# Optimization experiments

Measured on AMD Instinct MI355X. Metric: run time of the kernel, lower is better.

Reference implementation:

```python
import jax, jax.numpy as jnp
import numpy as np

D_K = 64.0  # key size from init


def setup_inputs() -> dict:
    key = jax.random.key(0)
    k1, k2, k3, k4, k5 = jax.random.split(key, 5)
    B, H, S, D = 2, 16, 2048, 64
    q = jax.random.normal(k1, (B, H, S, D), dtype=jnp.float32)
    v = jax.random.normal(k2, (B, H, S, D), dtype=jnp.float32)
    k = jax.random.normal(k3, (B, H, S, D), dtype=jnp.float32)
    att_mask = jax.random.normal(k4, (B, 1, S, S), dtype=jnp.float32)
    seq_mask = jax.random.uniform(k5, (B, 1, 1, S), dtype=jnp.float32)
    return {"q": q, "v": v, "k": k, "att_mask": att_mask, "seq_mask": seq_mask}


def reference(q, v, k, att_mask, seq_mask):
    # scores: [B, H, S, S]
    scores = jnp.einsum("bhqd,bhkd->bhqk", q, k) / jnp.sqrt(jnp.asarray(D_K, q.dtype))
    scores = scores + att_mask
    weights = jax.nn.softmax(scores, axis=-1)
    weights = weights * seq_mask  # post-softmax mask, no renormalization
    out = jnp.einsum("bhqk,bhkd->bhqd", weights, v)
    return out
```

## Files before the change

### kernel.cpp

```cpp
#include <hip/hip_runtime.h>
#include <hip/hip_bf16.h>
#include <stdint.h>

typedef __attribute__((ext_vector_type(8)))  short    short8;
typedef __attribute__((ext_vector_type(4)))  float    floatx4;
typedef __attribute__((ext_vector_type(16))) float    floatx16;
typedef __attribute__((ext_vector_type(4)))  ushort   ushortx4;

static __device__ __forceinline__ ushort f2bf(float f) {
  union { float f; uint32_t u; } c;
  c.f = f;
  uint32_t u = c.u;
  uint32_t r = (u + 0x7FFFu + ((u >> 16) & 1u)) >> 16;
  return (ushort)r;
}

static __device__ __forceinline__ uint32_t pkbf(float a, float b) {
  return (uint32_t)f2bf(a) | ((uint32_t)f2bf(b) << 16);
}

static __device__ __forceinline__ short8 pack8(floatx4 a, floatx4 b) {
  short8 t;
  t[0] = (short)f2bf(a[0]); t[1] = (short)f2bf(a[1]);
  t[2] = (short)f2bf(a[2]); t[3] = (short)f2bf(a[3]);
  t[4] = (short)f2bf(b[0]); t[5] = (short)f2bf(b[1]);
  t[6] = (short)f2bf(b[2]); t[7] = (short)f2bf(b[3]);
  return t;
}

#define MFMA32(a, b, c) __builtin_amdgcn_mfma_f32_32x32x16_bf16((a), (b), (c), 0, 0, 0)

constexpr int S_LEN = 2048;
constexpr int DH    = 64;
constexpr int QBLK  = 128;
constexpr int KVBLK = 64;
constexpr int NT    = S_LEN / KVBLK;

static __device__ __forceinline__ void swap32(uint32_t& a, uint32_t& b, int hi) {
#if __has_builtin(__builtin_amdgcn_permlane32_swap)
  typedef int intx2 __attribute__((ext_vector_type(2)));
  intx2 r = __builtin_amdgcn_permlane32_swap((int)a, (int)b, false, false);
  a = (uint32_t)r[0]; b = (uint32_t)r[1];
#else
  uint32_t pa = (uint32_t)__shfl_xor((int)a, 32, 64);
  uint32_t pb = (uint32_t)__shfl_xor((int)b, 32, 64);
  uint32_t na = hi ? pb : a;
  uint32_t nb = hi ? b  : pa;
  a = na; b = nb;
#endif
}

__global__ __launch_bounds__(256, 2)
void attn_fwd(const float* __restrict__ Q, const float* __restrict__ V,
              const float* __restrict__ K, const float* __restrict__ AM,
              const float* __restrict__ SM, float* __restrict__ O)
{
  __shared__ ushort Kl[2][KVBLK * DH];
  __shared__ ushort Vt[2][DH * KVBLK];
  __shared__ float  smlds[S_LEN];

  const int bh   = blockIdx.x;
  const int qt   = blockIdx.y;
  const int tid  = threadIdx.x;
  const int lane = tid & 63;
  const int wave = tid >> 6;
  const int l31  = lane & 31;
  const int hi   = lane >> 5;

  const float* qptr  = Q  + (size_t)bh * S_LEN * DH;
  const float* kptr  = K  + (size_t)bh * S_LEN * DH;
  const float* vptr  = V  + (size_t)bh * S_LEN * DH;
  const float* amptr = AM + (size_t)(bh >> 4) * S_LEN * S_LEN;
  const float* smptr = SM + (size_t)(bh >> 4) * S_LEN;
  float* optr = O + (size_t)bh * S_LEN * DH;

  for (int i = tid; i < S_LEN / 4; i += 256)
    ((floatx4*)smlds)[i] = ((const floatx4*)smptr)[i];

  const int qw = qt * QBLK + wave * 32;

  short8 qf[4];
  {
    const float* p = qptr + (size_t)(qw + l31) * DH + hi * 8;
    #pragma unroll
    for (int s = 0; s < 4; ++s) {
      floatx4 f0 = *(const floatx4*)(p + s * 16);
      floatx4 f1 = *(const floatx4*)(p + s * 16 + 4);
      qf[s] = pack8(f0, f1);
    }
  }

  const int krow = tid >> 2;
  const int kcol = (tid & 3) * 16;
  const int kcb  = (tid & 3) * 2;
  const int vr0  = (tid & 15) * 4;
  const int vd0  = (tid >> 4) * 4;

  floatx4 kreg[4], vreg[4];
  floatx4 amreg[2][4], amnx[2][4];

  auto LOADKV = [&](int t) {
    const float* kg = kptr + (size_t)(t * KVBLK + krow) * DH + kcol;
    #pragma unroll
    for (int j = 0; j < 4; ++j) kreg[j] = ((const floatx4*)kg)[j];
    #pragma unroll
    for (int i = 0; i < 4; ++i)
      vreg[i] = *(const floatx4*)(vptr + (size_t)(t * KVBLK + vr0 + i) * DH + vd0);
  };

  auto WRITEKV = [&](int c) {
    const int sw = krow & 7;
    *(short8*)&Kl[c][krow * 64 + ((kcb ^ sw) * 8)]       = pack8(kreg[0], kreg[1]);
    *(short8*)&Kl[c][krow * 64 + (((kcb + 1) ^ sw) * 8)] = pack8(kreg[2], kreg[3]);
    #pragma unroll
    for (int d = 0; d < 4; ++d) {
      ushortx4 w;
      w[0] = f2bf(vreg[0][d]); w[1] = f2bf(vreg[1][d]);
      w[2] = f2bf(vreg[2][d]); w[3] = f2bf(vreg[3][d]);
      const int row = vd0 + d;
      const int ch  = (vr0 >> 3) ^ (row & 7);
      *(ushortx4*)&Vt[c][row * 64 + ch * 8 + (vr0 & 7)] = w;
    }
  };

  auto LOADAM = [&](int t, floatx4 am[2][4]) {
    const float* base = amptr + (size_t)(qw + l31) * S_LEN + t * KVBLK + hi * 4;
    #pragma unroll
    for (int blk = 0; blk < 2; ++blk)
      #pragma unroll
      for (int j = 0; j < 4; ++j)
        am[blk][j] = *(const floatx4*)(base + blk * 32 + j * 8);
  };

  LOADKV(0);
  WRITEKV(0);
  LOADAM(0, amreg);

  float m_run = -3.0e38f, l_run = 0.f;
  floatx16 oacc[2];
  #pragma unroll
  for (int db = 0; db < 2; ++db)
    #pragma unroll
    for (int r = 0; r < 16; ++r) oacc[db][r] = 0.f;

  #pragma unroll 1
  for (int t = 0; t < NT; ++t) {
    const int c = t & 1;
    __syncthreads();

    floatx16 sacc[2];
    #pragma unroll
    for (int blk = 0; blk < 2; ++blk) {
      #pragma unroll
      for (int r = 0; r < 16; ++r) sacc[blk][r] = 0.f;
      const int row = blk * 32 + l31;
      const int sw  = row & 7;
      #pragma unroll
      for (int s = 0; s < 4; ++s) {
        const int ch = (s * 2 + hi) ^ sw;
        short8 kf = *(const short8*)&Kl[c][row * 64 + ch * 8];
        sacc[blk] = MFMA32(kf, qf[s], sacc[blk]);
      }
    }

    float p[2][16];
    float pmax = -3.0e38f;
    #pragma unroll
    for (int blk = 0; blk < 2; ++blk)
      #pragma unroll
      for (int r = 0; r < 16; ++r) {
        const float v = fmaf(sacc[blk][r], 0.125f, amreg[blk][r >> 2][r & 3]);
        p[blk][r] = v;
        pmax = fmaxf(pmax, v);
      }
    pmax = fmaxf(pmax, __shfl_xor(pmax, 32, 64));

    if (__any(pmax > m_run)) {
      const float mnew = fmaxf(m_run, pmax);
      const float fac  = __expf(m_run - mnew);
      float fw[16];
      #pragma unroll
      for (int r = 0; r < 16; ++r)
        fw[r] = __shfl(fac, (r & 3) + 8 * (r >> 2) + 4 * hi, 64);
      #pragma unroll
      for (int db = 0; db < 2; ++db)
        #pragma unroll
        for (int r = 0; r < 16; ++r) oacc[db][r] *= fw[r];
      l_run *= fac;
      m_run = mnew;
    }

    float ssum = 0.f;
    #pragma unroll
    for (int blk = 0; blk < 2; ++blk)
      #pragma unroll
      for (int r = 0; r < 16; ++r) {
        const float e = __expf(p[blk][r] - m_run);
        p[blk][r] = e;
        ssum += e;
      }
    ssum += __shfl_xor(ssum, 32, 64);
    l_run += ssum;

    const bool pf = (t + 1 < NT);
    if (pf) { LOADKV(t + 1); LOADAM(t + 1, amnx); }

    floatx4 smv[2][4];
    #pragma unroll
    for (int blk = 0; blk < 2; ++blk)
      #pragma unroll
      for (int j = 0; j < 4; ++j)
        smv[blk][j] = *(const floatx4*)&smlds[t * KVBLK + blk * 32 + hi * 4 + j * 8];

    uint32_t pw[2][2][4];
    #pragma unroll
    for (int blk = 0; blk < 2; ++blk)
      #pragma unroll
      for (int ks = 0; ks < 2; ++ks) {
        float q0 = p[blk][ks * 8 + 0] * smv[blk][ks * 2 + 0][0];
        float q1 = p[blk][ks * 8 + 1] * smv[blk][ks * 2 + 0][1];
        float q2 = p[blk][ks * 8 + 2] * smv[blk][ks * 2 + 0][2];
        float q3 = p[blk][ks * 8 + 3] * smv[blk][ks * 2 + 0][3];
        float q4 = p[blk][ks * 8 + 4] * smv[blk][ks * 2 + 1][0];
        float q5 = p[blk][ks * 8 + 5] * smv[blk][ks * 2 + 1][1];
        float q6 = p[blk][ks * 8 + 6] * smv[blk][ks * 2 + 1][2];
        float q7 = p[blk][ks * 8 + 7] * smv[blk][ks * 2 + 1][3];
        uint32_t w0 = pkbf(q0, q1);
        uint32_t w1 = pkbf(q2, q3);
        uint32_t w2 = pkbf(q4, q5);
        uint32_t w3 = pkbf(q6, q7);
        swap32(w0, w2, hi);
        swap32(w1, w3, hi);
        pw[blk][ks][0] = w0; pw[blk][ks][1] = w1;
        pw[blk][ks][2] = w2; pw[blk][ks][3] = w3;
      }

    #pragma unroll
    for (int blk = 0; blk < 2; ++blk)
      #pragma unroll
      for (int ks = 0; ks < 2; ++ks) {
        union { uint32_t u[4]; short8 s; } af;
        af.u[0] = pw[blk][ks][0]; af.u[1] = pw[blk][ks][1];
        af.u[2] = pw[blk][ks][2]; af.u[3] = pw[blk][ks][3];
        #pragma unroll
        for (int db = 0; db < 2; ++db) {
          const int row = db * 32 + l31;
          const int ch  = (blk * 4 + ks * 2 + hi) ^ (row & 7);
          short8 vf = *(const short8*)&Vt[c][row * 64 + ch * 8];
          oacc[db] = MFMA32(af.s, vf, oacc[db]);
        }
      }

    if (pf) {
      WRITEKV(c ^ 1);
      #pragma unroll
      for (int blk = 0; blk < 2; ++blk)
        #pragma unroll
        for (int j = 0; j < 4; ++j) amreg[blk][j] = amnx[blk][j];
    }
  }

  const float inv = 1.0f / l_run;
  float iw[16];
  #pragma unroll
  for (int r = 0; r < 16; ++r)
    iw[r] = __shfl(inv, (r & 3) + 8 * (r >> 2) + 4 * hi, 64);
  #pragma unroll
  for (int db = 0; db < 2; ++db)
    #pragma unroll
    for (int r = 0; r < 16; ++r) {
      const int qr = (r & 3) + 8 * (r >> 2) + 4 * hi;
      optr[(size_t)(qw + qr) * DH + db * 32 + l31] = oacc[db][r] * iw[r];
    }
}

extern "C" void kernel_launch(void* const* d_in, const int* in_sizes, int n_in,
                              void* d_out, int out_size, void* d_ws, size_t ws_size,
                              hipStream_t stream) {
  const float* q  = (const float*)d_in[0];
  const float* v  = (const float*)d_in[1];
  const float* k  = (const float*)d_in[2];
  const float* am = (const float*)d_in[3];
  const float* sm = (const float*)d_in[4];
  float* o = (float*)d_out;

  dim3 grid(32, S_LEN / QBLK);
  attn_fwd<<<grid, 256, 0, stream>>>(q, v, k, am, sm, o);
}
```

Baseline: 117.5 us.

## Use hardware bf16 pack, ping-pong mask registers, and prioritize MFMA phases

Replaces the software round-to-nearest bf16 conversion with the v_cvt_pk_bf16_f32 instruction for Q, K, V and probability packing. The KV loop is unrolled by two with alternating attention-mask register sets, which removes the per-iteration register copy and the prefetch conditionals by clamping the last prefetch to a redundant reload. It also raises wave priority around the two MFMA blocks via s_setprio so matrix work is issued ahead of other waves. The trade-offs are a wasted final reload and write of the last K/V tile, and possibly more register pressure from the unrolled body.

```diff
diff --git a/kernel.cpp b/kernel.cpp
--- a/kernel.cpp
+++ b/kernel.cpp
@@ -5,27 +5,19 @@
 typedef __attribute__((ext_vector_type(8)))  short    short8;
 typedef __attribute__((ext_vector_type(4)))  float    floatx4;
 typedef __attribute__((ext_vector_type(16))) float    floatx16;
-typedef __attribute__((ext_vector_type(4)))  ushort   ushortx4;
-
-static __device__ __forceinline__ ushort f2bf(float f) {
-  union { float f; uint32_t u; } c;
-  c.f = f;
-  uint32_t u = c.u;
-  uint32_t r = (u + 0x7FFFu + ((u >> 16) & 1u)) >> 16;
-  return (ushort)r;
-}
-
-static __device__ __forceinline__ uint32_t pkbf(float a, float b) {
-  return (uint32_t)f2bf(a) | ((uint32_t)f2bf(b) << 16);
-}
-
-static __device__ __forceinline__ short8 pack8(floatx4 a, floatx4 b) {
-  short8 t;
-  t[0] = (short)f2bf(a[0]); t[1] = (short)f2bf(a[1]);
-  t[2] = (short)f2bf(a[2]); t[3] = (short)f2bf(a[3]);
-  t[4] = (short)f2bf(b[0]); t[5] = (short)f2bf(b[1]);
-  t[6] = (short)f2bf(b[2]); t[7] = (short)f2bf(b[3]);
-  return t;
+typedef __attribute__((ext_vector_type(2)))  uint32_t uintx2;
+
+static __device__ __forceinline__ uint32_t cvtpk(float lo, float hi) {
+  uint32_t r;
+  asm("v_cvt_pk_bf16_f32 %0, %1, %2" : "=v"(r) : "v"(lo), "v"(hi));
+  return r;
+}
+
+static __device__ __forceinline__ short8 pack8c(floatx4 a, floatx4 b) {
+  union { uint32_t u[4]; short8 s; } r;
+  r.u[0] = cvtpk(a[0], a[1]); r.u[1] = cvtpk(a[2], a[3]);
+  r.u[2] = cvtpk(b[0], b[1]); r.u[3] = cvtpk(b[2], b[3]);
+  return r.s;
 }
 
 #define MFMA32(a, b, c) __builtin_amdgcn_mfma_f32_32x32x16_bf16((a), (b), (c), 0, 0, 0)
@@ -86,7 +78,7 @@
     for (int s = 0; s < 4; ++s) {
       floatx4 f0 = *(const floatx4*)(p + s * 16);
       floatx4 f1 = *(const floatx4*)(p + s * 16 + 4);
-      qf[s] = pack8(f0, f1);
+      qf[s] = pack8c(f0, f1);
     }
   }
 
@@ -97,7 +89,7 @@
   const int vd0  = (tid >> 4) * 4;
 
   floatx4 kreg[4], vreg[4];
-  floatx4 amreg[2][4], amnx[2][4];
+  floatx4 amA[2][4], amB[2][4];
 
   auto LOADKV = [&](int t) {
     const float* kg = kptr + (size_t)(t * KVBLK + krow) * DH + kcol;
@@ -110,20 +102,20 @@
 
   auto WRITEKV = [&](int c) {
     const int sw = krow & 7;
-    *(short8*)&Kl[c][krow * 64 + ((kcb ^ sw) * 8)]       = pack8(kreg[0], kreg[1]);
-    *(short8*)&Kl[c][krow * 64 + (((kcb + 1) ^ sw) * 8)] = pack8(kreg[2], kreg[3]);
+    *(short8*)&Kl[c][krow * 64 + ((kcb ^ sw) * 8)]       = pack8c(kreg[0], kreg[1]);
+    *(short8*)&Kl[c][krow * 64 + (((kcb + 1) ^ sw) * 8)] = pack8c(kreg[2], kreg[3]);
     #pragma unroll
     for (int d = 0; d < 4; ++d) {
-      ushortx4 w;
-      w[0] = f2bf(vreg[0][d]); w[1] = f2bf(vreg[1][d]);
-      w[2] = f2bf(vreg[2][d]); w[3] = f2bf(vreg[3][d]);
+      uintx2 w;
+      w[0] = cvtpk(vreg[0][d], vreg[1][d]);
+      w[1] = cvtpk(vreg[2][d], vreg[3][d]);
       const int row = vd0 + d;
       const int ch  = (vr0 >> 3) ^ (row & 7);
-      *(ushortx4*)&Vt[c][row * 64 + ch * 8 + (vr0 & 7)] = w;
-    }
-  };
-
-  auto LOADAM = [&](int t, floatx4 am[2][4]) {
+      *(uintx2*)&Vt[c][row * 64 + ch * 8 + (vr0 & 7)] = w;
+    }
+  };
+
+  auto LOADAM = [&](int t, floatx4 (&am)[2][4]) {
     const float* base = amptr + (size_t)(qw + l31) * S_LEN + t * KVBLK + hi * 4;
     #pragma unroll
     for (int blk = 0; blk < 2; ++blk)
@@ -134,7 +126,7 @@
 
   LOADKV(0);
   WRITEKV(0);
-  LOADAM(0, amreg);
+  LOADAM(0, amA);
 
   float m_run = -3.0e38f, l_run = 0.f;
   floatx16 oacc[2];
@@ -143,12 +135,11 @@
     #pragma unroll
     for (int r = 0; r < 16; ++r) oacc[db][r] = 0.f;
 
-  #pragma unroll 1
-  for (int t = 0; t < NT; ++t) {
-    const int c = t & 1;
+  auto STEP = [&](int t, int c, floatx4 (&amC)[2][4], floatx4 (&amN)[2][4]) {
     __syncthreads();
 
     floatx16 sacc[2];
+    __builtin_amdgcn_s_setprio(1);
     #pragma unroll
     for (int blk = 0; blk < 2; ++blk) {
       #pragma unroll
@@ -162,6 +153,7 @@
         sacc[blk] = MFMA32(kf, qf[s], sacc[blk]);
       }
     }
+    __builtin_amdgcn_s_setprio(0);
 
     float p[2][16];
     float pmax = -3.0e38f;
@@ -169,7 +161,7 @@
     for (int blk = 0; blk < 2; ++blk)
       #pragma unroll
       for (int r = 0; r < 16; ++r) {
-        const float v = fmaf(sacc[blk][r], 0.125f, amreg[blk][r >> 2][r & 3]);
+        const float v = fmaf(sacc[blk][r], 0.125f, amC[blk][r >> 2][r & 3]);
         p[blk][r] = v;
         pmax = fmaxf(pmax, v);
       }
@@ -202,8 +194,9 @@
     ssum += __shfl_xor(ssum, 32, 64);
     l_run += ssum;
 
-    const bool pf = (t + 1 < NT);
-    if (pf) { LOADKV(t + 1); LOADAM(t + 1, amnx); }
+    const int tn = (t + 1 < NT) ? t + 1 : NT - 1;
+    LOADKV(tn);
+    LOADAM(tn, amN);
 
     floatx4 smv[2][4];
     #pragma unroll
@@ -217,24 +210,21 @@
     for (int blk = 0; blk < 2; ++blk)
       #pragma unroll
       for (int ks = 0; ks < 2; ++ks) {
-        float q0 = p[blk][ks * 8 + 0] * smv[blk][ks * 2 + 0][0];
-        float q1 = p[blk][ks * 8 + 1] * smv[blk][ks * 2 + 0][1];
-        float q2 = p[blk][ks * 8 + 2] * smv[blk][ks * 2 + 0][2];
-        float q3 = p[blk][ks * 8 + 3] * smv[blk][ks * 2 + 0][3];
-        float q4 = p[blk][ks * 8 + 4] * smv[blk][ks * 2 + 1][0];
-        float q5 = p[blk][ks * 8 + 5] * smv[blk][ks * 2 + 1][1];
-        float q6 = p[blk][ks * 8 + 6] * smv[blk][ks * 2 + 1][2];
-        float q7 = p[blk][ks * 8 + 7] * smv[blk][ks * 2 + 1][3];
-        uint32_t w0 = pkbf(q0, q1);
-        uint32_t w1 = pkbf(q2, q3);
-        uint32_t w2 = pkbf(q4, q5);
-        uint32_t w3 = pkbf(q6, q7);
+        uint32_t w0 = cvtpk(p[blk][ks * 8 + 0] * smv[blk][ks * 2 + 0][0],
+                            p[blk][ks * 8 + 1] * smv[blk][ks * 2 + 0][1]);
+        uint32_t w1 = cvtpk(p[blk][ks * 8 + 2] * smv[blk][ks * 2 + 0][2],
+                            p[blk][ks * 8 + 3] * smv[blk][ks * 2 + 0][3]);
+        uint32_t w2 = cvtpk(p[blk][ks * 8 + 4] * smv[blk][ks * 2 + 1][0],
+                            p[blk][ks * 8 + 5] * smv[blk][ks * 2 + 1][1]);
+        uint32_t w3 = cvtpk(p[blk][ks * 8 + 6] * smv[blk][ks * 2 + 1][2],
+                            p[blk][ks * 8 + 7] * smv[blk][ks * 2 + 1][3]);
         swap32(w0, w2, hi);
         swap32(w1, w3, hi);
         pw[blk][ks][0] = w0; pw[blk][ks][1] = w1;
         pw[blk][ks][2] = w2; pw[blk][ks][3] = w3;
       }
 
+    __builtin_amdgcn_s_setprio(1);
     #pragma unroll
     for (int blk = 0; blk < 2; ++blk)
       #pragma unroll
@@ -250,14 +240,15 @@
           oacc[db] = MFMA32(af.s, vf, oacc[db]);
         }
       }
-
-    if (pf) {
-      WRITEKV(c ^ 1);
-      #pragma unroll
-      for (int blk = 0; blk < 2; ++blk)
-        #pragma unroll
-        for (int j = 0; j < 4; ++j) amreg[blk][j] = amnx[blk][j];
-    }
+    __builtin_amdgcn_s_setprio(0);
+
+    WRITEKV(c ^ 1);
+  };
+
+  #pragma unroll 1
+  for (int t = 0; t < NT; t += 2) {
+    STEP(t,     0, amA, amB);
+    STEP(t + 1, 1, amB, amA);
   }
 
   const float inv = 1.0f / l_run;
```

Result: slower. 124.8 us (+6.3%).
